# Kernel optimization log

Hardware: AMD Instinct MI355X
Metric: run time of the kernel (lower is better)

The kernel has to match this reference:

```python
import jax, jax.numpy as jnp
import numpy as np

B, T, D, H, F = 2, 128, 256, 8, 64
C = H * F          # channels = 512
TEMB = 512         # time_embed_dim


def setup_inputs() -> dict:
    key = jax.random.key(0)
    ks = jax.random.split(key, 9)
    qk = jax.random.normal(ks[0], (B, D, H, T, F), jnp.float32)
    # integer-valued relative distances in [-(T-1), T-1], stored as float
    pairwise_distances = jax.random.randint(ks[1], (B, T, T), -(T - 1), T).astype(jnp.float32)
    temb = jax.random.normal(ks[2], (B, T, TEMB), jnp.float32)
    # linear layer params (note: original zero-inits w_out/b_out; we use random
    # values so the kernel correctness test is non-trivial)
    w_dist = jax.random.normal(ks[3], (C, 3), jnp.float32) / np.sqrt(3.0)
    b_dist = jax.random.normal(ks[4], (C,), jnp.float32) * 0.02
    w_time = jax.random.normal(ks[5], (C, TEMB), jnp.float32) / np.sqrt(TEMB)
    b_time = jax.random.normal(ks[6], (C,), jnp.float32) * 0.02
    w_out = jax.random.normal(ks[7], (C, C), jnp.float32) / np.sqrt(C)
    b_out = jax.random.normal(ks[8], (C,), jnp.float32) * 0.02
    return {"qk": qk, "pairwise_distances": pairwise_distances, "temb": temb,
            "w_dist": w_dist, "b_dist": b_dist, "w_time": w_time, "b_time": b_time,
            "w_out": w_out, "b_out": b_out}


def _rpe_net(pd, temb, w_dist, b_dist, w_time, b_time, w_out, b_out):
    # distance features: [B,T,T,3]
    dist_embs = jnp.stack([
        jnp.log1p(jnp.maximum(pd, 0.0)),
        jnp.log1p(jnp.maximum(-pd, 0.0)),
        (pd == 0).astype(pd.dtype),
    ], axis=-1)
    # [B,T,1,C] + [B,T,T,C]
    temb_emb = jnp.einsum('btk,ck->btc', temb, w_time) + b_time
    emb = temb_emb[:, :, None, :] + jnp.einsum('btsk,ck->btsc', dist_embs, w_dist) + b_dist
    r = jnp.einsum('btsc,oc->btso', jax.nn.silu(emb), w_out) + b_out
    return r.reshape(B, T, T, H, F)  # [B,T,S,H,F]


def reference(qk, pairwise_distances, temb, w_dist, b_dist, w_time, b_time, w_out, b_out):
    R = _rpe_net(pairwise_distances, temb, w_dist, b_dist, w_time, b_time, w_out, b_out)
    # mode == 'qk'
    return jnp.einsum('bdhtf,btshf->bdhts', qk, R)
```

## Files before the change

### kernel.cpp

```cpp
#include <hip/hip_runtime.h>
#include <hip/hip_bf16.h>
#include <math.h>

typedef __attribute__((ext_vector_type(8))) short short8;
typedef __attribute__((ext_vector_type(4))) float f32x4;

#define B_    2
#define T_    128
#define D_    256
#define H_    8
#define F_    64
#define C_    512
#define TEMB_ 512

static __device__ __forceinline__ unsigned short f2bf(float f) {
  __hip_bfloat16 h = __float2bfloat16(f);
  return reinterpret_cast<unsigned short&>(h);
}
static __device__ __forceinline__ unsigned int pk2(float a, float b) {
  return (unsigned int)f2bf(a) | ((unsigned int)f2bf(b) << 16);
}

__global__ __launch_bounds__(256) void k_prep(
    const float* __restrict__ w_out, const float* __restrict__ w_dist,
    short* __restrict__ wsw, float* __restrict__ wd4)
{
  int gid = blockIdx.x * 256 + threadIdx.x;
  for (int s = gid; s < 32768; s += 16384) {
    int oi = s >> 10, rem = s & 1023, kjg = rem >> 6, l = rem & 63;
    int o = oi * 16 + (l & 15), c = kjg * 32 + (l >> 4) * 8;
    const float* src = w_out + (size_t)o * C_ + c;
    float4 a = *reinterpret_cast<const float4*>(src);
    float4 b = *reinterpret_cast<const float4*>(src + 4);
    uint4 v; v.x = pk2(a.x, a.y); v.y = pk2(a.z, a.w);
    v.z = pk2(b.x, b.y); v.w = pk2(b.z, b.w);
    *reinterpret_cast<uint4*>(wsw + (size_t)s * 8) = v;
  }
  if (gid < C_) {
    wd4[gid * 4 + 0] = w_dist[gid * 3 + 0];
    wd4[gid * 4 + 1] = w_dist[gid * 3 + 1];
    wd4[gid * 4 + 2] = w_dist[gid * 3 + 2];
    wd4[gid * 4 + 3] = 0.f;
  }
}

__global__ __launch_bounds__(256) void k_base(
    const float* __restrict__ temb, const float* __restrict__ w_time,
    const float* __restrict__ b_time, const float* __restrict__ b_dist,
    float* __restrict__ base)
{
  __shared__ float tt[32][64];
  __shared__ float wt[64][65];
  const int bt0 = blockIdx.x * 32;
  const int c0  = blockIdx.y * 64;
  const int tid = threadIdx.x;
  const int cl  = tid & 63;
  const int g   = tid >> 6;
  float acc[8] = {0.f,0.f,0.f,0.f,0.f,0.f,0.f,0.f};

  for (int k0 = 0; k0 < TEMB_; k0 += 64) {
#pragma unroll
    for (int i = 0; i < 8; ++i) {
      int idx = tid + i * 256; int r = idx >> 6, k = idx & 63;
      tt[r][k] = temb[(size_t)(bt0 + r) * TEMB_ + k0 + k];
    }
#pragma unroll
    for (int i = 0; i < 16; ++i) {
      int idx = tid + i * 256; int r = idx >> 6, k = idx & 63;
      wt[r][k] = w_time[(size_t)(c0 + r) * TEMB_ + k0 + k];
    }
    __syncthreads();
#pragma unroll
    for (int k = 0; k < 64; ++k) {
      float w = wt[cl][k];
#pragma unroll
      for (int j = 0; j < 8; ++j) acc[j] += tt[g + 4 * j][k] * w;
    }
    __syncthreads();
  }
  float bb = b_time[c0 + cl] + b_dist[c0 + cl];
#pragma unroll
  for (int j = 0; j < 8; ++j)
    base[(size_t)(bt0 + g + 4 * j) * C_ + c0 + cl] = acc[j] + bb;
}

__global__ __launch_bounds__(256, 2) void k_rpe(
    const float* __restrict__ pd, const float* __restrict__ base,
    const float* __restrict__ wd4, const short* __restrict__ wsw,
    const float* __restrict__ b_out, unsigned short* __restrict__ R)
{
  __shared__ __align__(16) short At[8192];
  __shared__ __align__(16) short Bt[16384];
  __shared__ float df[3][T_];

  const int bx   = blockIdx.x;
  const int bt   = bx >> 1;
  const int half = bx & 1;
  const int b    = bt >> 7;
  const int t    = bt & 127;
  const int tid  = threadIdx.x;
  const int lane = tid & 63;
  const int wave = tid >> 6;
  const int wm   = wave >> 1;
  const int wn   = wave & 1;
  const int lanem = lane & 15;
  const int laneg = lane >> 4;

  if (tid < T_) {
    float p = pd[((size_t)b * T_ + t) * T_ + tid];
    df[0][tid] = log1pf(fmaxf(p, 0.f));
    df[1][tid] = log1pf(fmaxf(-p, 0.f));
    df[2][tid] = (p == 0.f) ? 1.f : 0.f;
  }

  const int s_low = tid & 15;
  const int cg    = (tid >> 4) & 7;
  const int si_b  = (tid >> 7) * 4;
  const int kjA   = cg >> 2;
  const int kgrp  = cg & 3;
  const int laneslotA = s_low + 16 * kgrp;
  const float* baserow = base + (size_t)bt * C_;

  f32x4 acc[4][8];
#pragma unroll
  for (int mi = 0; mi < 4; ++mi)
#pragma unroll
    for (int ni = 0; ni < 8; ++ni) acc[mi][ni] = (f32x4){0.f, 0.f, 0.f, 0.f};

  for (int kt = 0; kt < 8; ++kt) {
    __syncthreads();
#pragma unroll
    for (int i = 0; i < 8; ++i) {
      int idx  = i * 256 + tid;
      int oi_l = idx >> 7, kj = (idx >> 6) & 1, l = idx & 63;
      int gslot = ((half * 16 + oi_l) * 16 + kt * 2 + kj) * 64 + l;
      uint4 v = *reinterpret_cast<const uint4*>(wsw + (size_t)gslot * 8);
      *reinterpret_cast<uint4*>(&Bt[idx * 8]) = v;
    }
    {
      const int cglob = kt * 64 + cg * 8;
      float4 b0 = *reinterpret_cast<const float4*>(baserow + cglob);
      float4 b1 = *reinterpret_cast<const float4*>(baserow + cglob + 4);
      float bs[8] = {b0.x, b0.y, b0.z, b0.w, b1.x, b1.y, b1.z, b1.w};
      float4 w[8];
#pragma unroll
      for (int j = 0; j < 8; ++j)
        w[j] = *reinterpret_cast<const float4*>(wd4 + (size_t)(cglob + j) * 4);
#pragma unroll
      for (int q = 0; q < 4; ++q) {
        int si = si_b + q;
        int s  = si * 16 + s_low;
        float d0 = df[0][s], d1 = df[1][s], d2 = df[2][s];
        float sl[8];
#pragma unroll
        for (int j = 0; j < 8; ++j) {
          float x = bs[j] + d0 * w[j].x + d1 * w[j].y + d2 * w[j].z;
          sl[j] = x / (1.f + __expf(-x));
        }
        uint4 v; v.x = pk2(sl[0], sl[1]); v.y = pk2(sl[2], sl[3]);
        v.z = pk2(sl[4], sl[5]); v.w = pk2(sl[6], sl[7]);
        *reinterpret_cast<uint4*>(&At[((si * 2 + kjA) * 64 + laneslotA) * 8]) = v;
      }
    }
    __syncthreads();
#pragma unroll
    for (int kj = 0; kj < 2; ++kj) {
      short8 a[4];
#pragma unroll
      for (int mi = 0; mi < 4; ++mi)
        a[mi] = *reinterpret_cast<const short8*>(
            &At[(((wm * 4 + mi) * 2 + kj) * 64 + lane) * 8]);
#pragma unroll
      for (int ni = 0; ni < 8; ++ni) {
        short8 bb = *reinterpret_cast<const short8*>(
            &Bt[(((wn * 8 + ni) * 2 + kj) * 64 + lane) * 8]);
#pragma unroll
        for (int mi = 0; mi < 4; ++mi)
          acc[mi][ni] = __builtin_amdgcn_mfma_f32_16x16x32_bf16(
              a[mi], bb, acc[mi][ni], 0, 0, 0);
      }
    }
  }
  const int o_base = half * 256 + wn * 128;
#pragma unroll
  for (int ni = 0; ni < 8; ++ni) {
    int o = o_base + ni * 16 + lanem;
    float bo = b_out[o];
#pragma unroll
    for (int mi = 0; mi < 4; ++mi) {
      int s0 = wm * 64 + mi * 16 + laneg * 4;
#pragma unroll
      for (int reg = 0; reg < 4; ++reg)
        R[((size_t)bt * T_ + s0 + reg) * C_ + o] = f2bf(acc[mi][ni][reg] + bo);
    }
  }
}

__global__ __launch_bounds__(256, 2) void k_qkr(
    const float* __restrict__ qk, const unsigned short* __restrict__ R,
    float* __restrict__ out)
{
  const int bx = blockIdx.x;
  const int h  = bx & 7;
  const int t  = (bx >> 3) & 127;
  const int b  = bx >> 10;
  const int bt = b * T_ + t;
  const int tid  = threadIdx.x;
  const int lane = tid & 63;
  const int wave = tid >> 6;
  const int lanem = lane & 15;
  const int laneg = lane >> 4;
  const int d0w = wave * 64;

  const float* qkb = qk + (size_t)b * D_ * H_ * T_ * F_
                        + (size_t)h * T_ * F_ + (size_t)t * F_;
  const unsigned short* Rb = R + (size_t)bt * T_ * C_ + h * F_;

  f32x4 acc[4][8];
#pragma unroll
  for (int mi = 0; mi < 4; ++mi)
#pragma unroll
    for (int ni = 0; ni < 8; ++ni) acc[mi][ni] = (f32x4){0.f, 0.f, 0.f, 0.f};

#pragma unroll
  for (int kj = 0; kj < 2; ++kj) {
    const int f0 = kj * 32 + laneg * 8;
    short8 a[4];
#pragma unroll
    for (int mi = 0; mi < 4; ++mi) {
      const float* src = qkb + (size_t)(d0w + mi * 16 + lanem) * (H_ * T_ * F_) + f0;
      float4 q0 = *reinterpret_cast<const float4*>(src);
      float4 q1 = *reinterpret_cast<const float4*>(src + 4);
      union { uint4 u; short8 s; } cv;
      cv.u.x = pk2(q0.x, q0.y); cv.u.y = pk2(q0.z, q0.w);
      cv.u.z = pk2(q1.x, q1.y); cv.u.w = pk2(q1.z, q1.w);
      a[mi] = cv.s;
    }
#pragma unroll
    for (int ni = 0; ni < 8; ++ni) {
      short8 bb = *reinterpret_cast<const short8*>(
          Rb + (size_t)(ni * 16 + lanem) * C_ + f0);
#pragma unroll
      for (int mi = 0; mi < 4; ++mi)
        acc[mi][ni] = __builtin_amdgcn_mfma_f32_16x16x32_bf16(
            a[mi], bb, acc[mi][ni], 0, 0, 0);
    }
  }

  float* outb = out + (size_t)b * D_ * H_ * T_ * T_
                    + (size_t)h * T_ * T_ + (size_t)t * T_;
#pragma unroll
  for (int mi = 0; mi < 4; ++mi) {
#pragma unroll
    for (int reg = 0; reg < 4; ++reg) {
      int d = d0w + mi * 16 + laneg * 4 + reg;
      float* row = outb + (size_t)d * (H_ * T_ * T_);
#pragma unroll
      for (int ni = 0; ni < 8; ++ni)
        row[ni * 16 + lanem] = acc[mi][ni][reg];
    }
  }
}

extern "C" void kernel_launch(void* const* d_in, const int* in_sizes, int n_in,
                              void* d_out, int out_size, void* d_ws, size_t ws_size,
                              hipStream_t stream) {
  const float* qk     = (const float*)d_in[0];
  const float* pd     = (const float*)d_in[1];
  const float* temb   = (const float*)d_in[2];
  const float* w_dist = (const float*)d_in[3];
  const float* b_dist = (const float*)d_in[4];
  const float* w_time = (const float*)d_in[5];
  const float* b_time = (const float*)d_in[6];
  const float* w_out  = (const float*)d_in[7];
  const float* b_out  = (const float*)d_in[8];
  float* out = (float*)d_out;

  char* ws = (char*)d_ws;
  float* base          = (float*)(ws);
  float* wd4           = (float*)(ws + 524288);
  short* wsw           = (short*)(ws + 532480);
  unsigned short* Rbuf = (unsigned short*)(ws + 1056768);

  hipLaunchKernelGGL(k_prep, dim3(64), dim3(256), 0, stream,
                     w_out, w_dist, wsw, wd4);
  hipLaunchKernelGGL(k_base, dim3(8, 8), dim3(256), 0, stream,
                     temb, w_time, b_time, b_dist, base);
  hipLaunchKernelGGL(k_rpe, dim3(512), dim3(256), 0, stream,
                     pd, base, wd4, wsw, b_out, Rbuf);
  hipLaunchKernelGGL(k_qkr, dim3(B_ * T_ * H_), dim3(256), 0, stream,
                     qk, Rbuf, out);
}
```

Measured before the change: 195.2 us.

## Fuse RPE MLP and qk contraction into one kernel with R kept in LDS

Merges the R-generation GEMM and the qk·R contraction into a single 512-thread kernel per (b,t). The full 128x512 bf16 R tile (128KB) stays in XOR-swizzled shared memory, so the global R round-trip (64MB written and reread) disappears. w_out fragments now go straight from global memory into registers instead of being staged through shared memory. The qk loads in the second phase are double-buffered. The trade-offs are a large LDS footprint (~145KB) that allows only one block per CU despite launch_bounds(512,2), and only 256 blocks across the GPU.

```diff
diff --git a/kernel.cpp b/kernel.cpp
--- a/kernel.cpp
+++ b/kernel.cpp
@@ -84,25 +84,22 @@
     base[(size_t)(bt0 + g + 4 * j) * C_ + c0 + cl] = acc[j] + bb;
 }
 
-__global__ __launch_bounds__(256, 2) void k_rpe(
-    const float* __restrict__ pd, const float* __restrict__ base,
-    const float* __restrict__ wd4, const short* __restrict__ wsw,
-    const float* __restrict__ b_out, unsigned short* __restrict__ R)
+__global__ __launch_bounds__(512, 2) void k_fused(
+    const float* __restrict__ qk, const float* __restrict__ pd,
+    const float* __restrict__ base, const float* __restrict__ wd4,
+    const short* __restrict__ wsw, const float* __restrict__ b_out,
+    float* __restrict__ out)
 {
+  __shared__ __align__(16) unsigned short Rlds[T_ * C_];
   __shared__ __align__(16) short At[8192];
-  __shared__ __align__(16) short Bt[16384];
   __shared__ float df[3][T_];
 
-  const int bx   = blockIdx.x;
-  const int bt   = bx >> 1;
-  const int half = bx & 1;
-  const int b    = bt >> 7;
-  const int t    = bt & 127;
+  const int bt = blockIdx.x;
+  const int b  = bt >> 7;
+  const int t  = bt & 127;
   const int tid  = threadIdx.x;
   const int lane = tid & 63;
   const int wave = tid >> 6;
-  const int wm   = wave >> 1;
-  const int wn   = wave & 1;
   const int lanem = lane & 15;
   const int laneg = lane >> 4;
 
@@ -113,12 +110,15 @@
     df[2][tid] = (p == 0.f) ? 1.f : 0.f;
   }
 
+  const int wm = wave >> 2;
+  const int wn = wave & 3;
+
   const int s_low = tid & 15;
   const int cg    = (tid >> 4) & 7;
-  const int si_b  = (tid >> 7) * 4;
+  const int si_b  = (tid >> 7) * 2;
   const int kjA   = cg >> 2;
-  const int kgrp  = cg & 3;
-  const int laneslotA = s_low + 16 * kgrp;
+  const int cgl   = cg & 3;
+  const int laneslotA = s_low + 16 * cgl;
   const float* baserow = base + (size_t)bt * C_;
 
   f32x4 acc[4][8];
@@ -129,25 +129,23 @@
 
   for (int kt = 0; kt < 8; ++kt) {
     __syncthreads();
-#pragma unroll
-    for (int i = 0; i < 8; ++i) {
-      int idx  = i * 256 + tid;
-      int oi_l = idx >> 7, kj = (idx >> 6) & 1, l = idx & 63;
-      int gslot = ((half * 16 + oi_l) * 16 + kt * 2 + kj) * 64 + l;
-      uint4 v = *reinterpret_cast<const uint4*>(wsw + (size_t)gslot * 8);
-      *reinterpret_cast<uint4*>(&Bt[idx * 8]) = v;
-    }
+    short8 b0[8], b1[8];
+    const int kjg0 = kt * 2, kjg1 = kt * 2 + 1;
+#pragma unroll
+    for (int ni = 0; ni < 8; ++ni)
+      b0[ni] = *reinterpret_cast<const short8*>(
+          wsw + ((size_t)((wn * 8 + ni) * 16 + kjg0) * 64 + lane) * 8);
     {
       const int cglob = kt * 64 + cg * 8;
-      float4 b0 = *reinterpret_cast<const float4*>(baserow + cglob);
-      float4 b1 = *reinterpret_cast<const float4*>(baserow + cglob + 4);
-      float bs[8] = {b0.x, b0.y, b0.z, b0.w, b1.x, b1.y, b1.z, b1.w};
+      float4 bv0 = *reinterpret_cast<const float4*>(baserow + cglob);
+      float4 bv1 = *reinterpret_cast<const float4*>(baserow + cglob + 4);
+      float bs[8] = {bv0.x, bv0.y, bv0.z, bv0.w, bv1.x, bv1.y, bv1.z, bv1.w};
       float4 w[8];
 #pragma unroll
       for (int j = 0; j < 8; ++j)
         w[j] = *reinterpret_cast<const float4*>(wd4 + (size_t)(cglob + j) * 4);
 #pragma unroll
-      for (int q = 0; q < 4; ++q) {
+      for (int q = 0; q < 2; ++q) {
         int si = si_b + q;
         int s  = si * 16 + s_low;
         float d0 = df[0][s], d1 = df[1][s], d2 = df[2][s];
@@ -162,103 +160,121 @@
         *reinterpret_cast<uint4*>(&At[((si * 2 + kjA) * 64 + laneslotA) * 8]) = v;
       }
     }
+#pragma unroll
+    for (int ni = 0; ni < 8; ++ni)
+      b1[ni] = *reinterpret_cast<const short8*>(
+          wsw + ((size_t)((wn * 8 + ni) * 16 + kjg1) * 64 + lane) * 8);
     __syncthreads();
-#pragma unroll
-    for (int kj = 0; kj < 2; ++kj) {
-      short8 a[4];
-#pragma unroll
-      for (int mi = 0; mi < 4; ++mi)
-        a[mi] = *reinterpret_cast<const short8*>(
-            &At[(((wm * 4 + mi) * 2 + kj) * 64 + lane) * 8]);
-#pragma unroll
-      for (int ni = 0; ni < 8; ++ni) {
-        short8 bb = *reinterpret_cast<const short8*>(
-            &Bt[(((wn * 8 + ni) * 2 + kj) * 64 + lane) * 8]);
-#pragma unroll
-        for (int mi = 0; mi < 4; ++mi)
-          acc[mi][ni] = __builtin_amdgcn_mfma_f32_16x16x32_bf16(
-              a[mi], bb, acc[mi][ni], 0, 0, 0);
-      }
-    }
-  }
-  const int o_base = half * 256 + wn * 128;
-#pragma unroll
-  for (int ni = 0; ni < 8; ++ni) {
-    int o = o_base + ni * 16 + lanem;
-    float bo = b_out[o];
-#pragma unroll
-    for (int mi = 0; mi < 4; ++mi) {
-      int s0 = wm * 64 + mi * 16 + laneg * 4;
-#pragma unroll
-      for (int reg = 0; reg < 4; ++reg)
-        R[((size_t)bt * T_ + s0 + reg) * C_ + o] = f2bf(acc[mi][ni][reg] + bo);
-    }
-  }
-}
-
-__global__ __launch_bounds__(256, 2) void k_qkr(
-    const float* __restrict__ qk, const unsigned short* __restrict__ R,
-    float* __restrict__ out)
-{
-  const int bx = blockIdx.x;
-  const int h  = bx & 7;
-  const int t  = (bx >> 3) & 127;
-  const int b  = bx >> 10;
-  const int bt = b * T_ + t;
-  const int tid  = threadIdx.x;
-  const int lane = tid & 63;
-  const int wave = tid >> 6;
-  const int lanem = lane & 15;
-  const int laneg = lane >> 4;
-  const int d0w = wave * 64;
-
-  const float* qkb = qk + (size_t)b * D_ * H_ * T_ * F_
-                        + (size_t)h * T_ * F_ + (size_t)t * F_;
-  const unsigned short* Rb = R + (size_t)bt * T_ * C_ + h * F_;
-
-  f32x4 acc[4][8];
-#pragma unroll
-  for (int mi = 0; mi < 4; ++mi)
-#pragma unroll
-    for (int ni = 0; ni < 8; ++ni) acc[mi][ni] = (f32x4){0.f, 0.f, 0.f, 0.f};
-
-#pragma unroll
-  for (int kj = 0; kj < 2; ++kj) {
-    const int f0 = kj * 32 + laneg * 8;
-    short8 a[4];
-#pragma unroll
-    for (int mi = 0; mi < 4; ++mi) {
-      const float* src = qkb + (size_t)(d0w + mi * 16 + lanem) * (H_ * T_ * F_) + f0;
-      float4 q0 = *reinterpret_cast<const float4*>(src);
-      float4 q1 = *reinterpret_cast<const float4*>(src + 4);
-      union { uint4 u; short8 s; } cv;
-      cv.u.x = pk2(q0.x, q0.y); cv.u.y = pk2(q0.z, q0.w);
-      cv.u.z = pk2(q1.x, q1.y); cv.u.w = pk2(q1.z, q1.w);
-      a[mi] = cv.s;
-    }
-#pragma unroll
-    for (int ni = 0; ni < 8; ++ni) {
-      short8 bb = *reinterpret_cast<const short8*>(
-          Rb + (size_t)(ni * 16 + lanem) * C_ + f0);
+    short8 a0[4], a1[4];
+#pragma unroll
+    for (int mi = 0; mi < 4; ++mi)
+      a0[mi] = *reinterpret_cast<const short8*>(
+          &At[(((wm * 4 + mi) * 2 + 0) * 64 + lane) * 8]);
+#pragma unroll
+    for (int ni = 0; ni < 8; ++ni)
 #pragma unroll
       for (int mi = 0; mi < 4; ++mi)
         acc[mi][ni] = __builtin_amdgcn_mfma_f32_16x16x32_bf16(
-            a[mi], bb, acc[mi][ni], 0, 0, 0);
-    }
-  }
-
-  float* outb = out + (size_t)b * D_ * H_ * T_ * T_
-                    + (size_t)h * T_ * T_ + (size_t)t * T_;
-#pragma unroll
-  for (int mi = 0; mi < 4; ++mi) {
-#pragma unroll
-    for (int reg = 0; reg < 4; ++reg) {
-      int d = d0w + mi * 16 + laneg * 4 + reg;
-      float* row = outb + (size_t)d * (H_ * T_ * T_);
+            a0[mi], b0[ni], acc[mi][ni], 0, 0, 0);
+#pragma unroll
+    for (int mi = 0; mi < 4; ++mi)
+      a1[mi] = *reinterpret_cast<const short8*>(
+          &At[(((wm * 4 + mi) * 2 + 1) * 64 + lane) * 8]);
+#pragma unroll
+    for (int ni = 0; ni < 8; ++ni)
+#pragma unroll
+      for (int mi = 0; mi < 4; ++mi)
+        acc[mi][ni] = __builtin_amdgcn_mfma_f32_16x16x32_bf16(
+            a1[mi], b1[ni], acc[mi][ni], 0, 0, 0);
+  }
+
+#pragma unroll
+  for (int ni = 0; ni < 8; ++ni) {
+    const int o  = wn * 128 + ni * 16 + lanem;
+    const float bo = b_out[o];
+    const int g  = o >> 3;
+#pragma unroll
+    for (int mi = 0; mi < 4; ++mi) {
+#pragma unroll
+      for (int reg = 0; reg < 4; ++reg) {
+        int s  = wm * 64 + mi * 16 + laneg * 4 + reg;
+        int gp = (g & ~7) | ((g ^ s) & 7);
+        Rlds[s * 512 + gp * 8 + (o & 7)] = f2bf(acc[mi][ni][reg] + bo);
+      }
+    }
+  }
+  __syncthreads();
+
+  const int h = wave;
+  short8 brf[2][8];
+#pragma unroll
+  for (int kj = 0; kj < 2; ++kj)
+#pragma unroll
+    for (int ni = 0; ni < 8; ++ni) {
+      int s  = ni * 16 + lanem;
+      int g  = h * 8 + kj * 4 + laneg;
+      int gp = (g & ~7) | ((g ^ s) & 7);
+      brf[kj][ni] = *reinterpret_cast<const short8*>(&Rlds[s * 512 + gp * 8]);
+    }
+
+  const int HTF = H_ * T_ * F_;
+  const int HTT = H_ * T_ * T_;
+  const float* qkb = qk + (size_t)b * D_ * HTF + (size_t)h * T_ * F_ + (size_t)t * F_;
+  float* outb = out + (size_t)b * D_ * HTT + (size_t)h * T_ * T_ + (size_t)t * T_;
+
+  auto LOADC = [&](int d0, float4* buf) {
+#pragma unroll
+    for (int mi = 0; mi < 2; ++mi) {
+      const float* src = qkb + (size_t)(d0 + mi * 16 + lanem) * HTF + laneg * 8;
+      buf[mi * 4 + 0] = *reinterpret_cast<const float4*>(src);
+      buf[mi * 4 + 1] = *reinterpret_cast<const float4*>(src + 4);
+      buf[mi * 4 + 2] = *reinterpret_cast<const float4*>(src + 32);
+      buf[mi * 4 + 3] = *reinterpret_cast<const float4*>(src + 36);
+    }
+  };
+  auto COMP = [&](int d0, const float4* buf) {
+    f32x4 ac[2][8];
+#pragma unroll
+    for (int mi = 0; mi < 2; ++mi)
+#pragma unroll
+      for (int ni = 0; ni < 8; ++ni) ac[mi][ni] = (f32x4){0.f, 0.f, 0.f, 0.f};
+#pragma unroll
+    for (int kj = 0; kj < 2; ++kj) {
+      short8 av[2];
+#pragma unroll
+      for (int mi = 0; mi < 2; ++mi) {
+        float4 p0 = buf[mi * 4 + kj * 2], p1 = buf[mi * 4 + kj * 2 + 1];
+        union { uint4 u; short8 s; } cv;
+        cv.u.x = pk2(p0.x, p0.y); cv.u.y = pk2(p0.z, p0.w);
+        cv.u.z = pk2(p1.x, p1.y); cv.u.w = pk2(p1.z, p1.w);
+        av[mi] = cv.s;
+      }
 #pragma unroll
       for (int ni = 0; ni < 8; ++ni)
-        row[ni * 16 + lanem] = acc[mi][ni][reg];
-    }
+#pragma unroll
+        for (int mi = 0; mi < 2; ++mi)
+          ac[mi][ni] = __builtin_amdgcn_mfma_f32_16x16x32_bf16(
+              av[mi], brf[kj][ni], ac[mi][ni], 0, 0, 0);
+    }
+#pragma unroll
+    for (int mi = 0; mi < 2; ++mi)
+#pragma unroll
+      for (int reg = 0; reg < 4; ++reg) {
+        float* row = outb + (size_t)(d0 + mi * 16 + laneg * 4 + reg) * HTT;
+#pragma unroll
+        for (int ni = 0; ni < 8; ++ni)
+          row[ni * 16 + lanem] = ac[mi][ni][reg];
+      }
+  };
+
+  float4 bufA[8], bufB[8];
+  LOADC(0, bufA);
+#pragma unroll
+  for (int cc = 0; cc < 4; ++cc) {
+    LOADC(cc * 64 + 32, bufB);
+    COMP(cc * 64, bufA);
+    if (cc < 3) LOADC(cc * 64 + 64, bufA);
+    COMP(cc * 64 + 32, bufB);
   }
 }
 
@@ -277,17 +293,14 @@
   float* out = (float*)d_out;
 
   char* ws = (char*)d_ws;
-  float* base          = (float*)(ws);
-  float* wd4           = (float*)(ws + 524288);
-  short* wsw           = (short*)(ws + 532480);
-  unsigned short* Rbuf = (unsigned short*)(ws + 1056768);
+  float* base = (float*)(ws);
+  float* wd4  = (float*)(ws + 524288);
+  short* wsw  = (short*)(ws + 532480);
 
   hipLaunchKernelGGL(k_prep, dim3(64), dim3(256), 0, stream,
                      w_out, w_dist, wsw, wd4);
   hipLaunchKernelGGL(k_base, dim3(8, 8), dim3(256), 0, stream,
                      temb, w_time, b_time, b_dist, base);
-  hipLaunchKernelGGL(k_rpe, dim3(512), dim3(256), 0, stream,
-                     pd, base, wd4, wsw, b_out, Rbuf);
-  hipLaunchKernelGGL(k_qkr, dim3(B_ * T_ * H_), dim3(256), 0, stream,
-                     qk, Rbuf, out);
-}
+  hipLaunchKernelGGL(k_fused, dim3(B_ * T_), dim3(512), 0, stream,
+                     qk, pd, base, wd4, wsw, b_out, out);
+}
```

Measured after the change: 174.7 us. 1.12x faster.
